# Kernel tuning notes

Measured on AMD Instinct MI355X. Metric: run time of the kernel, lower is better.

Reference implementation:

```python
import jax, jax.numpy as jnp
import numpy as np

N, E, H, C = 100000, 800000, 128, 26


def setup_inputs() -> dict:
    key = jax.random.key(0)
    ks = jax.random.split(key, 12)
    s = 0.05
    return {
        "node_feat": jax.random.normal(ks[0], (N, H), jnp.float32),
        "descriptor": jax.random.normal(ks[1], (N, H), jnp.float32),
        "sub_idx": jax.random.randint(ks[2], (E,), 0, N, jnp.int32),
        "obj_idx": jax.random.randint(ks[3], (E,), 0, N, jnp.int32),
        "We": jax.random.normal(ks[4], (2 * H, H), jnp.float32) * s,
        "be": jnp.zeros((H,), jnp.float32),
        "Wq": jax.random.normal(ks[5], (2 * H, H), jnp.float32) * s,
        "bq": jnp.zeros((H,), jnp.float32),
        "Wk": jax.random.normal(ks[6], (2 * H, H), jnp.float32) * s,
        "bk": jnp.zeros((H,), jnp.float32),
        "Wv": jax.random.normal(ks[7], (2 * H, H), jnp.float32) * s,
        "bv": jnp.zeros((H,), jnp.float32),
        "Wc1": jax.random.normal(ks[8], (H, H // 2), jnp.float32) * s,
        "bc1": jnp.zeros((H // 2,), jnp.float32),
        "Wc2": jax.random.normal(ks[9], (H // 2, H // 4), jnp.float32) * s,
        "bc2": jnp.zeros((H // 4,), jnp.float32),
        "Wc3": jax.random.normal(ks[10], (H // 4, C), jnp.float32) * s,
        "bc3": jnp.zeros((C,), jnp.float32),
    }


def reference(node_feat, descriptor, sub_idx, obj_idx,
              We, be, Wq, bq, Wk, bk, Wv, bv,
              Wc1, bc1, Wc2, bc2, Wc3, bc3):
    # Gather edge endpoint features (irregular access), concat -> [E, 2H]
    geo = jnp.concatenate([node_feat[sub_idx], node_feat[obj_idx]], axis=1)
    non_geo = jnp.concatenate([descriptor[sub_idx], descriptor[obj_idx]], axis=1)

    origin = geo @ We + be          # edge_lin
    query = geo @ Wq + bq
    key = non_geo @ Wk + bk
    value = non_geo @ Wv + bv

    # elementwise q*k then softmax over feature dim (dim=1 in torch)
    alpha = jax.nn.softmax(query * key, axis=1)
    fused = value * alpha + origin  # [E, H]

    # classifier: Linear+ReLU, Linear (no ReLU), Linear(->classes)
    h = jax.nn.relu(fused @ Wc1 + bc1)
    h = h @ Wc2 + bc2
    out = h @ Wc3 + bc3             # [E, C]
    return out
```

## Files before the change

kernel.cpp:

```cpp
#include <hip/hip_runtime.h>
#include <hip/hip_bf16.h>

typedef short short8 __attribute__((ext_vector_type(8)));
typedef float f32x4 __attribute__((ext_vector_type(4)));

#define NEDGE 800000
#define HD    128
#define TM    64
#define LDA   264
#define LDF   136
#define LDH1  72
#define LDH2  40

__device__ __forceinline__ unsigned short f2bf(float f) {
    unsigned int u = __float_as_uint(f);
    unsigned int r = u + 0x7fffu + ((u >> 16) & 1u);
    return (unsigned short)(r >> 16);
}
__device__ __forceinline__ float bf2f(unsigned short u) {
    union { unsigned int i; float f; } v; v.i = ((unsigned int)u) << 16; return v.f;
}
__device__ __forceinline__ unsigned int pk_bf16(float a, float b) {
    __hip_bfloat162 h = __float22bfloat162_rn(make_float2(a, b));
    union { __hip_bfloat162 h2; unsigned int u; } c; c.h2 = h; return c.u;
}

__global__ void pack_all(const float* __restrict__ We, const float* __restrict__ Wq,
                         const float* __restrict__ Wk, const float* __restrict__ Wv,
                         const float* __restrict__ Wc1, const float* __restrict__ Wc2,
                         const float* __restrict__ Wc3,
                         unsigned short* __restrict__ ws) {
    int b = blockIdx.x;
    const float* src; unsigned short* dst; int KT, NT, ncols;
    if (b < 512) {
        int sel = b >> 7;
        src = sel == 0 ? We : sel == 1 ? Wq : sel == 2 ? Wk : Wv;
        dst = ws + sel * 32768;
        KT = 8; NT = 8; ncols = 128; b &= 127;
    } else if (b < 544) { src = Wc1; dst = ws + 131072; KT = 4; NT = 4; ncols = 64; b -= 512; }
    else if (b < 552)   { src = Wc2; dst = ws + 139264; KT = 2; NT = 2; ncols = 32; b -= 544; }
    else                { src = Wc3; dst = ws + 141312; KT = 1; NT = 2; ncols = 26; b -= 552; }
    int idx = b * 256 + threadIdx.x;
    int total = NT * KT * 64 * 8;
    if (idx >= total) return;
    int j = idx & 7;
    int l = (idx >> 3) & 63;
    int rem = idx >> 9;
    int s = rem % KT;
    int t = rem / KT;
    int k = s * 32 + ((l >> 4) << 3) + j;
    int n = t * 16 + (l & 15);
    dst[idx] = (n < ncols) ? f2bf(src[k * ncols + n]) : (unsigned short)0;
}

__global__ __launch_bounds__(256, 4)
void fused_relcls(const float* __restrict__ nf,
                  const float* __restrict__ desc,
                  const int* __restrict__ sub, const int* __restrict__ obj,
                  const unsigned short* __restrict__ wef, const unsigned short* __restrict__ wqf,
                  const unsigned short* __restrict__ wkf, const unsigned short* __restrict__ wvf,
                  const unsigned short* __restrict__ wc1f, const unsigned short* __restrict__ wc2f,
                  const unsigned short* __restrict__ wc3f,
                  const float* __restrict__ be, const float* __restrict__ bq,
                  const float* __restrict__ bk, const float* __restrict__ bv,
                  const float* __restrict__ bc1, const float* __restrict__ bc2,
                  const float* __restrict__ bc3,
                  float* __restrict__ out)
{
    __shared__ __align__(16) unsigned short Abuf[TM * LDA];
    __shared__ float ssm[TM * 4];
    unsigned short* h1Buf = Abuf + 8704;
    unsigned short* h2Buf = Abuf + 13312;

    const int t  = threadIdx.x;
    const int w  = t >> 6;
    const int l  = t & 63;
    const int cl = l & 15;
    const int cq = l >> 4;
    const long e0 = (long)blockIdx.x * TM;
    const int wu = __builtin_amdgcn_readfirstlane(w);
    const int half = l >> 5;
    const int ci   = l & 31;

    {
        #pragma unroll
        for (int i = 0; i < 16; ++i) {
            int e = wu + 4 * i;
            int si = sub[e0 + e];
            int oi = obj[e0 + e];
            int idx = half ? oi : si;
            f32x4 v = *(const f32x4*)(nf + (long)idx * HD + ci * 4);
            uint2 o;
            o.x = pk_bf16(v[0], v[1]);
            o.y = pk_bf16(v[2], v[3]);
            *(uint2*)&Abuf[e * LDA + half * HD + ci * 4] = o;
        }
    }
    __syncthreads();

    f32x4 acc0[4][2], acc1[4][2];
    unsigned int opk[16];

    {
        float b0 = be[w * 32 + cl], b1 = be[w * 32 + 16 + cl];
        #pragma unroll
        for (int m = 0; m < 4; ++m) {
            acc0[m][0] = (f32x4){b0, b0, b0, b0};
            acc0[m][1] = (f32x4){b1, b1, b1, b1};
        }
        #pragma unroll
        for (int ks = 0; ks < 8; ++ks) {
            short8 a[4];
            #pragma unroll
            for (int m = 0; m < 4; ++m)
                a[m] = *(const short8*)&Abuf[(m * 16 + cl) * LDA + ks * 32 + cq * 8];
            short8 bw[2];
            #pragma unroll
            for (int tt = 0; tt < 2; ++tt)
                bw[tt] = *(const short8*)&wef[(((w * 2 + tt) * 8 + ks) * 64 + l) * 8];
            #pragma unroll
            for (int m = 0; m < 4; ++m)
                #pragma unroll
                for (int tt = 0; tt < 2; ++tt)
                    acc0[m][tt] = __builtin_amdgcn_mfma_f32_16x16x32_bf16(a[m], bw[tt], acc0[m][tt], 0, 0, 0);
        }
        #pragma unroll
        for (int m = 0; m < 4; ++m)
            #pragma unroll
            for (int tt = 0; tt < 2; ++tt) {
                opk[m * 4 + tt * 2 + 0] = pk_bf16(acc0[m][tt][0], acc0[m][tt][1]);
                opk[m * 4 + tt * 2 + 1] = pk_bf16(acc0[m][tt][2], acc0[m][tt][3]);
            }
    }

    {
        float b0 = bq[w * 32 + cl], b1 = bq[w * 32 + 16 + cl];
        #pragma unroll
        for (int m = 0; m < 4; ++m) {
            acc0[m][0] = (f32x4){b0, b0, b0, b0};
            acc0[m][1] = (f32x4){b1, b1, b1, b1};
        }
        #pragma unroll
        for (int ks = 0; ks < 8; ++ks) {
            short8 a[4];
            #pragma unroll
            for (int m = 0; m < 4; ++m)
                a[m] = *(const short8*)&Abuf[(m * 16 + cl) * LDA + ks * 32 + cq * 8];
            short8 bw[2];
            #pragma unroll
            for (int tt = 0; tt < 2; ++tt)
                bw[tt] = *(const short8*)&wqf[(((w * 2 + tt) * 8 + ks) * 64 + l) * 8];
            #pragma unroll
            for (int m = 0; m < 4; ++m)
                #pragma unroll
                for (int tt = 0; tt < 2; ++tt)
                    acc0[m][tt] = __builtin_amdgcn_mfma_f32_16x16x32_bf16(a[m], bw[tt], acc0[m][tt], 0, 0, 0);
        }
    }
    __syncthreads();

    {
        #pragma unroll
        for (int i = 0; i < 16; ++i) {
            int e = wu + 4 * i;
            int si = sub[e0 + e];
            int oi = obj[e0 + e];
            int idx = half ? oi : si;
            f32x4 v = *(const f32x4*)(desc + (long)idx * HD + ci * 4);
            uint2 o;
            o.x = pk_bf16(v[0], v[1]);
            o.y = pk_bf16(v[2], v[3]);
            *(uint2*)&Abuf[e * LDA + half * HD + ci * 4] = o;
        }
    }
    __syncthreads();

    {
        float b0 = bk[w * 32 + cl], b1 = bk[w * 32 + 16 + cl];
        #pragma unroll
        for (int m = 0; m < 4; ++m) {
            acc1[m][0] = (f32x4){b0, b0, b0, b0};
            acc1[m][1] = (f32x4){b1, b1, b1, b1};
        }
        #pragma unroll
        for (int ks = 0; ks < 8; ++ks) {
            short8 a[4];
            #pragma unroll
            for (int m = 0; m < 4; ++m)
                a[m] = *(const short8*)&Abuf[(m * 16 + cl) * LDA + ks * 32 + cq * 8];
            short8 bw[2];
            #pragma unroll
            for (int tt = 0; tt < 2; ++tt)
                bw[tt] = *(const short8*)&wkf[(((w * 2 + tt) * 8 + ks) * 64 + l) * 8];
            #pragma unroll
            for (int m = 0; m < 4; ++m)
                #pragma unroll
                for (int tt = 0; tt < 2; ++tt)
                    acc1[m][tt] = __builtin_amdgcn_mfma_f32_16x16x32_bf16(a[m], bw[tt], acc1[m][tt], 0, 0, 0);
        }
        #pragma unroll
        for (int m = 0; m < 4; ++m)
            #pragma unroll
            for (int tt = 0; tt < 2; ++tt)
                acc0[m][tt] *= acc1[m][tt];
    }

    {
        #pragma unroll
        for (int m = 0; m < 4; ++m) {
            float es[4];
            #pragma unroll
            for (int r = 0; r < 4; ++r) {
                float s = __expf(acc0[m][0][r]) + __expf(acc0[m][1][r]);
                s += __shfl_xor(s, 1);
                s += __shfl_xor(s, 2);
                s += __shfl_xor(s, 4);
                s += __shfl_xor(s, 8);
                es[r] = s;
            }
            if (cl == 0) {
                #pragma unroll
                for (int r = 0; r < 4; ++r)
                    ssm[(m * 16 + cq * 4 + r) * 4 + w] = es[r];
            }
        }
    }

    {
        float b0 = bv[w * 32 + cl], b1 = bv[w * 32 + 16 + cl];
        #pragma unroll
        for (int m = 0; m < 4; ++m) {
            acc1[m][0] = (f32x4){b0, b0, b0, b0};
            acc1[m][1] = (f32x4){b1, b1, b1, b1};
        }
        #pragma unroll
        for (int ks = 0; ks < 8; ++ks) {
            short8 a[4];
            #pragma unroll
            for (int m = 0; m < 4; ++m)
                a[m] = *(const short8*)&Abuf[(m * 16 + cl) * LDA + ks * 32 + cq * 8];
            short8 bw[2];
            #pragma unroll
            for (int tt = 0; tt < 2; ++tt)
                bw[tt] = *(const short8*)&wvf[(((w * 2 + tt) * 8 + ks) * 64 + l) * 8];
            #pragma unroll
            for (int m = 0; m < 4; ++m)
                #pragma unroll
                for (int tt = 0; tt < 2; ++tt)
                    acc1[m][tt] = __builtin_amdgcn_mfma_f32_16x16x32_bf16(a[m], bw[tt], acc1[m][tt], 0, 0, 0);
        }
    }
    __syncthreads();

    {
        unsigned short* fusedBuf = Abuf;
        #pragma unroll
        for (int m = 0; m < 4; ++m)
            #pragma unroll
            for (int r = 0; r < 4; ++r) {
                int row = m * 16 + cq * 4 + r;
                f32x4 b = *(const f32x4*)&ssm[row * 4];
                float inv = 1.0f / (b[0] + b[1] + b[2] + b[3]);
                #pragma unroll
                for (int tt = 0; tt < 2; ++tt) {
                    unsigned int word = opk[m * 4 + tt * 2 + (r >> 1)];
                    unsigned short us = (r & 1) ? (unsigned short)(word >> 16) : (unsigned short)(word & 0xffffu);
                    float Oval = bf2f(us);
                    float alpha = __expf(acc0[m][tt][r]) * inv;
                    float f = acc1[m][tt][r] * alpha + Oval;
                    fusedBuf[row * LDF + w * 32 + tt * 16 + cl] = f2bf(f);
                }
            }
    }
    __syncthreads();

    {
        const unsigned short* fusedBuf = Abuf;
        float b1 = bc1[w * 16 + cl];
        f32x4 acc[4];
        #pragma unroll
        for (int m = 0; m < 4; ++m) acc[m] = (f32x4){b1, b1, b1, b1};
        #pragma unroll
        for (int ks = 0; ks < 4; ++ks) {
            short8 a[4];
            #pragma unroll
            for (int m = 0; m < 4; ++m)
                a[m] = *(const short8*)&fusedBuf[(m * 16 + cl) * LDF + ks * 32 + cq * 8];
            short8 bw = *(const short8*)&wc1f[((w * 4 + ks) * 64 + l) * 8];
            #pragma unroll
            for (int m = 0; m < 4; ++m)
                acc[m] = __builtin_amdgcn_mfma_f32_16x16x32_bf16(a[m], bw, acc[m], 0, 0, 0);
        }
        #pragma unroll
        for (int m = 0; m < 4; ++m)
            #pragma unroll
            for (int r = 0; r < 4; ++r)
                h1Buf[(m * 16 + cq * 4 + r) * LDH1 + w * 16 + cl] = f2bf(fmaxf(acc[m][r], 0.f));
    }
    __syncthreads();

    {
        int tn = w & 1, mh = w >> 1;
        float b2 = bc2[tn * 16 + cl];
        f32x4 acc[2];
        acc[0] = (f32x4){b2, b2, b2, b2};
        acc[1] = (f32x4){b2, b2, b2, b2};
        #pragma unroll
        for (int ks = 0; ks < 2; ++ks) {
            short8 a[2];
            #pragma unroll
            for (int mm = 0; mm < 2; ++mm)
                a[mm] = *(const short8*)&h1Buf[((mh * 2 + mm) * 16 + cl) * LDH1 + ks * 32 + cq * 8];
            short8 bw = *(const short8*)&wc2f[((tn * 2 + ks) * 64 + l) * 8];
            #pragma unroll
            for (int mm = 0; mm < 2; ++mm)
                acc[mm] = __builtin_amdgcn_mfma_f32_16x16x32_bf16(a[mm], bw, acc[mm], 0, 0, 0);
        }
        #pragma unroll
        for (int mm = 0; mm < 2; ++mm)
            #pragma unroll
            for (int r = 0; r < 4; ++r)
                h2Buf[((mh * 2 + mm) * 16 + cq * 4 + r) * LDH2 + tn * 16 + cl] = f2bf(acc[mm][r]);
    }
    __syncthreads();

    {
        f32x4 acc[2];
        #pragma unroll
        for (int tt = 0; tt < 2; ++tt) {
            int col = tt * 16 + cl;
            float b3 = (col < 26) ? bc3[col] : 0.f;
            acc[tt] = (f32x4){b3, b3, b3, b3};
        }
        short8 a = *(const short8*)&h2Buf[(w * 16 + cl) * LDH2 + cq * 8];
        #pragma unroll
        for (int tt = 0; tt < 2; ++tt)
            acc[tt] = __builtin_amdgcn_mfma_f32_16x16x32_bf16(a, *(const short8*)&wc3f[(tt * 64 + l) * 8], acc[tt], 0, 0, 0);
        #pragma unroll
        for (int tt = 0; tt < 2; ++tt) {
            int col = tt * 16 + cl;
            if (col < 26) {
                #pragma unroll
                for (int r = 0; r < 4; ++r) {
                    long row = e0 + w * 16 + cq * 4 + r;
                    out[row * 26 + col] = acc[tt][r];
                }
            }
        }
    }
}

extern "C" void kernel_launch(void* const* d_in, const int* in_sizes, int n_in,
                              void* d_out, int out_size, void* d_ws, size_t ws_size,
                              hipStream_t stream) {
    const float* nf   = (const float*)d_in[0];
    const float* desc = (const float*)d_in[1];
    const int* sub = (const int*)d_in[2];
    const int* obj = (const int*)d_in[3];
    const float* We  = (const float*)d_in[4];
    const float* be  = (const float*)d_in[5];
    const float* Wq  = (const float*)d_in[6];
    const float* bq  = (const float*)d_in[7];
    const float* Wk  = (const float*)d_in[8];
    const float* bk  = (const float*)d_in[9];
    const float* Wv  = (const float*)d_in[10];
    const float* bv  = (const float*)d_in[11];
    const float* Wc1 = (const float*)d_in[12];
    const float* bc1 = (const float*)d_in[13];
    const float* Wc2 = (const float*)d_in[14];
    const float* bc2 = (const float*)d_in[15];
    const float* Wc3 = (const float*)d_in[16];
    const float* bc3 = (const float*)d_in[17];

    unsigned short* ws = (unsigned short*)d_ws;
    unsigned short* wef  = ws;
    unsigned short* wqf  = ws + 32768;
    unsigned short* wkf  = ws + 65536;
    unsigned short* wvf  = ws + 98304;
    unsigned short* wc1f = ws + 131072;
    unsigned short* wc2f = ws + 139264;
    unsigned short* wc3f = ws + 141312;

    pack_all<<<556, 256, 0, stream>>>(We, Wq, Wk, Wv, Wc1, Wc2, Wc3, ws);

    fused_relcls<<<NEDGE / TM, 256, 0, stream>>>(
        nf, desc, sub, obj,
        wef, wqf, wkf, wvf, wc1f, wc2f, wc3f,
        be, bq, bk, bv, bc1, bc2, bc3,
        (float*)d_out);
}
```

Before: 555.4 us.

## Pre-convert node tables to bf16 and prefetch descriptor gathers early

Result: slower. 596.8 us (+7.5%).

```diff
diff --git a/kernel.cpp b/kernel.cpp
--- a/kernel.cpp
+++ b/kernel.cpp
@@ -3,8 +3,10 @@
 
 typedef short short8 __attribute__((ext_vector_type(8)));
 typedef float f32x4 __attribute__((ext_vector_type(4)));
+typedef unsigned int uint4v __attribute__((ext_vector_type(4)));
 
 #define NEDGE 800000
+#define NNODE 100000
 #define HD    128
 #define TM    64
 #define LDA   264
@@ -12,6 +14,10 @@
 #define LDH1  72
 #define LDH2  40
 
+#define WOFF_NFB   142336
+#define WOFF_DESCB (142336 + 12800000)
+#define WS_NEED    ((size_t)(142336 + 2 * 12800000) * 2)
+
 __device__ __forceinline__ unsigned short f2bf(float f) {
     unsigned int u = __float_as_uint(f);
     unsigned int r = u + 0x7fffu + ((u >> 16) & 1u);
@@ -25,12 +31,29 @@
     union { __hip_bfloat162 h2; unsigned int u; } c; c.h2 = h; return c.u;
 }
 
-__global__ void pack_all(const float* __restrict__ We, const float* __restrict__ Wq,
-                         const float* __restrict__ Wk, const float* __restrict__ Wv,
-                         const float* __restrict__ Wc1, const float* __restrict__ Wc2,
-                         const float* __restrict__ Wc3,
-                         unsigned short* __restrict__ ws) {
+__global__ void pack_convert(const float* __restrict__ We, const float* __restrict__ Wq,
+                             const float* __restrict__ Wk, const float* __restrict__ Wv,
+                             const float* __restrict__ Wc1, const float* __restrict__ Wc2,
+                             const float* __restrict__ Wc3,
+                             const float* __restrict__ nf, const float* __restrict__ desc,
+                             unsigned short* __restrict__ ws) {
     int b = blockIdx.x;
+    if (b >= 556) {
+        int cb = b - 556;
+        const float* src; unsigned short* dst;
+        if (cb < 6250) { src = nf;   dst = ws + WOFF_NFB; }
+        else           { src = desc; dst = ws + WOFF_DESCB; cb -= 6250; }
+        long i = ((long)cb * 256 + threadIdx.x) * 8;
+        f32x4 v0 = *(const f32x4*)(src + i);
+        f32x4 v1 = *(const f32x4*)(src + i + 4);
+        uint4v o;
+        o.x = pk_bf16(v0[0], v0[1]);
+        o.y = pk_bf16(v0[2], v0[3]);
+        o.z = pk_bf16(v1[0], v1[1]);
+        o.w = pk_bf16(v1[2], v1[3]);
+        *(uint4v*)(dst + i) = o;
+        return;
+    }
     const float* src; unsigned short* dst; int KT, NT, ncols;
     if (b < 512) {
         int sel = b >> 7;
@@ -53,10 +76,12 @@
     dst[idx] = (n < ncols) ? f2bf(src[k * ncols + n]) : (unsigned short)0;
 }
 
+template<bool TAB>
 __global__ __launch_bounds__(256, 4)
 void fused_relcls(const float* __restrict__ nf,
                   const float* __restrict__ desc,
                   const int* __restrict__ sub, const int* __restrict__ obj,
+                  const unsigned short* __restrict__ nfb, const unsigned short* __restrict__ descb,
                   const unsigned short* __restrict__ wef, const unsigned short* __restrict__ wqf,
                   const unsigned short* __restrict__ wkf, const unsigned short* __restrict__ wvf,
                   const unsigned short* __restrict__ wc1f, const unsigned short* __restrict__ wc2f,
@@ -82,7 +107,28 @@
     const int half = l >> 5;
     const int ci   = l & 31;
 
-    {
+    uint2 dreg[16];
+
+    if constexpr (TAB) {
+        uint2 g[16];
+        #pragma unroll
+        for (int i = 0; i < 16; ++i) {
+            int e = wu + 4 * i;
+            int idx = half ? obj[e0 + e] : sub[e0 + e];
+            g[i] = *(const uint2*)(nfb + (long)idx * HD + ci * 4);
+        }
+        #pragma unroll
+        for (int i = 0; i < 16; ++i) {
+            int e = wu + 4 * i;
+            int idx = half ? obj[e0 + e] : sub[e0 + e];
+            dreg[i] = *(const uint2*)(descb + (long)idx * HD + ci * 4);
+        }
+        #pragma unroll
+        for (int i = 0; i < 16; ++i) {
+            int e = wu + 4 * i;
+            *(uint2*)&Abuf[e * LDA + half * HD + ci * 4] = g[i];
+        }
+    } else {
         #pragma unroll
         for (int i = 0; i < 16; ++i) {
             int e = wu + 4 * i;
@@ -159,7 +205,13 @@
     }
     __syncthreads();
 
-    {
+    if constexpr (TAB) {
+        #pragma unroll
+        for (int i = 0; i < 16; ++i) {
+            int e = wu + 4 * i;
+            *(uint2*)&Abuf[e * LDA + half * HD + ci * 4] = dreg[i];
+        }
+    } else {
         #pragma unroll
         for (int i = 0; i < 16; ++i) {
             int e = wu + 4 * i;
@@ -211,7 +263,11 @@
             float es[4];
             #pragma unroll
             for (int r = 0; r < 4; ++r) {
-                float s = __expf(acc0[m][0][r]) + __expf(acc0[m][1][r]);
+                float ea = __expf(acc0[m][0][r]);
+                float eb = __expf(acc0[m][1][r]);
+                acc0[m][0][r] = ea;
+                acc0[m][1][r] = eb;
+                float s = ea + eb;
                 s += __shfl_xor(s, 1);
                 s += __shfl_xor(s, 2);
                 s += __shfl_xor(s, 4);
@@ -266,7 +322,7 @@
                     unsigned int word = opk[m * 4 + tt * 2 + (r >> 1)];
                     unsigned short us = (r & 1) ? (unsigned short)(word >> 16) : (unsigned short)(word & 0xffffu);
                     float Oval = bf2f(us);
-                    float alpha = __expf(acc0[m][tt][r]) * inv;
+                    float alpha = acc0[m][tt][r] * inv;
                     float f = acc1[m][tt][r] * alpha + Oval;
                     fusedBuf[row * LDF + w * 32 + tt * 16 + cl] = f2bf(f);
                 }
@@ -336,16 +392,27 @@
         #pragma unroll
         for (int tt = 0; tt < 2; ++tt)
             acc[tt] = __builtin_amdgcn_mfma_f32_16x16x32_bf16(a, *(const short8*)&wc3f[(tt * 64 + l) * 8], acc[tt], 0, 0, 0);
+        float* ostg = (float*)Abuf;
         #pragma unroll
         for (int tt = 0; tt < 2; ++tt) {
             int col = tt * 16 + cl;
             if (col < 26) {
                 #pragma unroll
-                for (int r = 0; r < 4; ++r) {
-                    long row = e0 + w * 16 + cq * 4 + r;
-                    out[row * 26 + col] = acc[tt][r];
-                }
+                for (int r = 0; r < 4; ++r)
+                    ostg[(w * 16 + cq * 4 + r) * 26 + col] = acc[tt][r];
             }
+        }
+    }
+    __syncthreads();
+
+    {
+        const uint4v* src = (const uint4v*)Abuf;
+        uint4v* dst = (uint4v*)(out + e0 * 26);
+        #pragma unroll
+        for (int k2 = 0; k2 < 2; ++k2) {
+            int idx = t + k2 * 256;
+            if (idx < 416)
+                dst[idx] = src[idx];
         }
     }
 }
@@ -380,12 +447,25 @@
     unsigned short* wc1f = ws + 131072;
     unsigned short* wc2f = ws + 139264;
     unsigned short* wc3f = ws + 141312;
-
-    pack_all<<<556, 256, 0, stream>>>(We, Wq, Wk, Wv, Wc1, Wc2, Wc3, ws);
-
-    fused_relcls<<<NEDGE / TM, 256, 0, stream>>>(
-        nf, desc, sub, obj,
-        wef, wqf, wkf, wvf, wc1f, wc2f, wc3f,
-        be, bq, bk, bv, bc1, bc2, bc3,
-        (float*)d_out);
-}
+    unsigned short* nfb   = ws + WOFF_NFB;
+    unsigned short* descb = ws + WOFF_DESCB;
+
+    const bool tab = (ws_size >= WS_NEED);
+    const int prep_grid = tab ? 13056 : 556;
+
+    pack_convert<<<prep_grid, 256, 0, stream>>>(We, Wq, Wk, Wv, Wc1, Wc2, Wc3, nf, desc, ws);
+
+    if (tab) {
+        fused_relcls<true><<<NEDGE / TM, 256, 0, stream>>>(
+            nf, desc, sub, obj, nfb, descb,
+            wef, wqf, wkf, wvf, wc1f, wc2f, wc3f,
+            be, bq, bk, bv, bc1, bc2, bc3,
+            (float*)d_out);
+    } else {
+        fused_relcls<false><<<NEDGE / TM, 256, 0, stream>>>(
+            nf, desc, sub, obj, nfb, descb,
+            wef, wqf, wkf, wvf, wc1f, wc2f, wc3f,
+            be, bq, bk, bv, bc1, bc2, bc3,
+            (float*)d_out);
+    }
+}
```
